# Kernel tuning notes

Hardware: AMD Instinct MI355X
Metric: run time of the kernel (lower is better)

## Reference

```python
import jax, jax.numpy as jnp
import numpy as np

NMS_RADIUS = 2.0   # cfgs.NMS_radius (meters)
EPS = 1e-6         # torch nn.PairwiseDistance default eps (added to the diff)
M = 16384          # number of keypoint candidates
SCENE = 100.0      # scene extent in meters


def setup_inputs() -> dict:
    key = jax.random.key(0)
    k1, k2 = jax.random.split(key)
    nodes = jax.random.uniform(k1, (M, 3), dtype=jnp.float32) * SCENE
    overlap_score = jax.random.normal(k2, (M,), dtype=jnp.float32)
    return {"nodes": nodes, "overlap_score": overlap_score}


def _greedy_nms(nodes, radius):
    """Sequential greedy NMS: keep node i iff its distance to every
    already-kept node exceeds radius. Faithful to the torch loop:
    (dis > radius).sum() == n_kept  <=>  all kept dists > radius."""
    n = nodes.shape[0]

    def body(i, mask):
        # torch nn.PairwiseDistance computes ||x1 - x2 + eps||_2
        d = jnp.linalg.norm(nodes[i] - nodes + EPS, axis=-1)  # [n]
        keep = jnp.all(jnp.where(mask, d > radius, True))
        return mask.at[i].set(keep)

    mask0 = jnp.zeros(n, dtype=bool).at[0].set(True)
    return jax.lax.fori_loop(1, n, body, mask0)


def reference(nodes, overlap_score):
    # sort by overlap score descending, run greedy NMS, unsort the mask
    order = jnp.argsort(-overlap_score)
    mask_sorted = _greedy_nms(nodes[order], NMS_RADIUS)
    mask = jnp.zeros_like(mask_sorted).at[order].set(mask_sorted)
    nms_length = mask.sum(dtype=jnp.int32)[None]
    return mask, nms_length
```

## Files before the change

kernel.cpp:

```cpp
#include <hip/hip_runtime.h>


#define M_PTS    16384
#define RADIUS   2.0f
#define EPS_D    1e-6f
#define GRID_N   25
#define NCELLS   (GRID_N * GRID_N * GRID_N)
#define CELL_CAP 12
#define K_NBR    12
#define EPT      5
#define ACT_PAD  (EPT * 1024)


__device__ __forceinline__ int cell_of(float v) {
  int c = (int)(v * 0.25f);
  return c < 0 ? 0 : (c > GRID_N - 1 ? GRID_N - 1 : c);
}

__global__ __launch_bounds__(256) void zero_kernel(int4* __restrict__ p) {
  int i = blockIdx.x * 256 + threadIdx.x;
  if (i < 8003) p[i] = make_int4(0, 0, 0, 0);
}

__global__ __launch_bounds__(256) void grid_build(
    const float* __restrict__ nodes, const float* __restrict__ score,
    float4* __restrict__ pts, int* __restrict__ cell_cnt,
    unsigned short* __restrict__ cell_list) {
  int i = blockIdx.x * 256 + threadIdx.x;
  if (i >= M_PTS) return;
  float4 p;
  p.x = nodes[3 * i + 0];
  p.y = nodes[3 * i + 1];
  p.z = nodes[3 * i + 2];
  p.w = score[i];
  pts[i] = p;
  int cid = (cell_of(p.x) * GRID_N + cell_of(p.y)) * GRID_N + cell_of(p.z);
  int pos = atomicAdd(&cell_cnt[cid], 1);
  if (pos < CELL_CAP) cell_list[cid * CELL_CAP + pos] = (unsigned short)i;
}

__global__ __launch_bounds__(256) void nbr_scan(
    const float4* __restrict__ pts, const int* __restrict__ cell_cnt,
    const unsigned short* __restrict__ cell_list,
    int* __restrict__ cnt, unsigned short* __restrict__ nbr) {
  int t = blockIdx.x * 256 + threadIdx.x;
  int i = t / 27;
  int d = t - i * 27;
  if (i >= M_PTS) return;
  const float4 pi = pts[i];
  int cx = cell_of(pi.x) + (d / 9) - 1;
  int cy = cell_of(pi.y) + ((d / 3) % 3) - 1;
  int cz = cell_of(pi.z) + (d % 3) - 1;
  if (cx < 0 || cx >= GRID_N || cy < 0 || cy >= GRID_N ||
      cz < 0 || cz >= GRID_N) return;
  int cid = (cx * GRID_N + cy) * GRID_N + cz;
  int m = cell_cnt[cid];
  if (m > CELL_CAP) m = CELL_CAP;
  for (int s = 0; s < m; ++s) {
    int j = cell_list[cid * CELL_CAP + s];
    float4 pj = pts[j];
    bool earlier = (pj.w > pi.w) || ((pj.w == pi.w) && (j < i));
    if (!earlier) continue;
    float ddx = __fadd_rn(__fsub_rn(pi.x, pj.x), EPS_D);
    float ddy = __fadd_rn(__fsub_rn(pi.y, pj.y), EPS_D);
    float ddz = __fadd_rn(__fsub_rn(pi.z, pj.z), EPS_D);
    float d2 = __fadd_rn(__fadd_rn(__fmul_rn(ddx, ddx), __fmul_rn(ddy, ddy)),
                         __fmul_rn(ddz, ddz));
    float dist = __fsqrt_rn(d2);
    if (!(dist > RADIUS)) {
      int pos = atomicAdd(&cnt[i], 1);
      if (pos < K_NBR) nbr[i * K_NBR + pos] = (unsigned short)j;
    }
  }
}

__global__ __launch_bounds__(1024) void solve_kernel(
    const int* __restrict__ cnt, const unsigned short* __restrict__ nbr,
    int* __restrict__ out, int out_size) {
  __shared__ unsigned char mask_[M_PTS];
  __shared__ unsigned int act[ACT_PAD];
  __shared__ int act_n, total;
  volatile unsigned char* mask = mask_;

  const int tid = threadIdx.x;
  const int lane = tid & 63;
  if (tid == 0) { act_n = 0; total = 0; }
  for (int a = tid; a < ACT_PAD; a += 1024) act[a] = 0u;
  __syncthreads();

  for (int k = tid; k < M_PTS; k += 1024) {
    mask_[k] = 1;
    int c = cnt[k];
    if (c > K_NBR) c = K_NBR;
    unsigned long long b = __ballot(c > 0);
    int wcnt = __popcll(b);
    int wbase = 0;
    if (lane == 0 && wcnt) wbase = atomicAdd(&act_n, wcnt);
    wbase = __shfl(wbase, 0, 64);
    if (c > 0) {
      int pos = wbase + __popcll(b & ((1ull << lane) - 1ull));
      if (pos < ACT_PAD) act[pos] = (unsigned)k | ((unsigned)c << 16);
    }
  }
  __syncthreads();
  const int na = act_n;
  const bool ok = (na <= ACT_PAD);

  unsigned ae[EPT];
  unsigned short r0[EPT], r1[EPT], r2[EPT];
#pragma unroll
  for (int e = 0; e < EPT; ++e) {
    unsigned v = act[tid + e * 1024];
    ae[e] = v;
    int k = (int)(v & 0xFFFFu);
    int c = (int)(v >> 16);
    const unsigned short* row = nbr + (size_t)k * K_NBR;
    r0[e] = (c > 0) ? row[0] : (unsigned short)0;
    r1[e] = (c > 1) ? row[1] : (unsigned short)0;
    r2[e] = (c > 2) ? row[2] : (unsigned short)0;
  }
  __syncthreads();

  if (ok) {
    for (int it = 0; it < 96; ++it) {
      int any = 0;
      int m0[EPT];
#pragma unroll
      for (int e = 0; e < EPT; ++e) m0[e] = (int)mask[r0[e]];
#pragma unroll
      for (int e = 0; e < EPT; ++e) {
        unsigned v = ae[e];
        int c = (int)(v >> 16);
        if (!c) continue;
        int k = (int)(v & 0xFFFFu);
        int kp = m0[e] ^ 1;
        if (c > 1) kp &= (int)mask[r1[e]] ^ 1;
        if (c > 2) kp &= (int)mask[r2[e]] ^ 1;
        if (c > 3) {
          const unsigned short* row = nbr + (size_t)k * K_NBR;
          for (int t = 3; t < c; ++t) kp &= (int)mask[row[t]] ^ 1;
        }
        if (kp != (int)mask[k]) { mask[k] = (unsigned char)kp; any = 1; }
      }
      if (__syncthreads_count(any) == 0) break;
    }
  } else {
    __shared__ int changed;
    for (int it = 0; it < 512; ++it) {
      if (tid == 0) changed = 0;
      __syncthreads();
      int any = 0;
      for (int k = tid; k < M_PTS; k += 1024) {
        int c = cnt[k]; if (c > K_NBR) c = K_NBR;
        if (!c) continue;
        int kp = 1;
        for (int t = 0; t < c; ++t) kp &= (int)mask[nbr[k * K_NBR + t]] ^ 1;
        if (kp != (int)mask[k]) { mask_[k] = (unsigned char)kp; any = 1; }
      }
      if (any) changed = 1;
      __syncthreads();
      if (!changed) break;
    }
  }
  __syncthreads();

  int ks = 0;
  for (int k = tid; k < M_PTS; k += 1024) {
    int m = (int)mask_[k];
    out[k] = m;
    ks += m;
  }
#pragma unroll
  for (int off = 32; off > 0; off >>= 1) ks += __shfl_down(ks, off, 64);
  if (lane == 0) atomicAdd(&total, ks);
  __syncthreads();
  if (tid == 0) out[out_size - 1] = total;
}

extern "C" void kernel_launch(void* const* d_in, const int* in_sizes, int n_in,
                              void* d_out, int out_size, void* d_ws, size_t ws_size,
                              hipStream_t stream) {
  const float* nodes = (const float*)d_in[0];
  const float* score = (const float*)d_in[1];
  int* out = (int*)d_out;

  char* ws = (char*)d_ws;
  float4* pts = (float4*)ws;
  int* cell_cnt = (int*)(ws + 262144);
  int* cnt = (int*)(ws + 324644);
  unsigned short* cell_list = (unsigned short*)(ws + 393216);
  unsigned short* nbr = (unsigned short*)(ws + 770048);

  zero_kernel<<<32, 256, 0, stream>>>((int4*)(ws + 262144));
  grid_build<<<64, 256, 0, stream>>>(nodes, score, pts, cell_cnt, cell_list);
  nbr_scan<<<1728, 256, 0, stream>>>(pts, cell_cnt, cell_list, cnt, nbr);
  solve_kernel<<<1, 1024, 0, stream>>>(cnt, nbr, out, out_size);
}
```

Baseline: 40.57 us.

## Fuse NMS pipeline into one cooperative kernel with grid syncs

Replaces the four launches (zero, grid build, neighbor scan, solve) with a single cooperative kernel of 256x512 threads that separates the phases with grid-wide syncs, removing launch gaps between kernels. Non-block-0 blocks write out[k]=1 for points that have no earlier neighbors, and block 0 solves and writes only the active points. Block 0 now holds 10 entries per thread over 512 threads. The multi-kernel path is kept as a fallback if the cooperative launch fails. Grid-sync cost and a lower-occupancy solve block may offset the launch savings.

Result: slower. 139.8 us (+244.7%).

```diff
diff --git a/kernel.cpp b/kernel.cpp
--- a/kernel.cpp
+++ b/kernel.cpp
@@ -1,4 +1,7 @@
 #include <hip/hip_runtime.h>
+#include <hip/hip_cooperative_groups.h>
+
+namespace cg = cooperative_groups;
 
 
 #define M_PTS    16384
@@ -8,14 +11,195 @@
 #define NCELLS   (GRID_N * GRID_N * GRID_N)
 #define CELL_CAP 12
 #define K_NBR    12
-#define EPT      5
-#define ACT_PAD  (EPT * 1024)
+#define NBLK     256
+#define NTHR     512
+#define EPT      10
+#define ACT_PAD  (EPT * NTHR)
+#define NTASK    (M_PTS * 27)
 
 
 __device__ __forceinline__ int cell_of(float v) {
   int c = (int)(v * 0.25f);
   return c < 0 ? 0 : (c > GRID_N - 1 ? GRID_N - 1 : c);
 }
+
+__device__ __forceinline__ bool edge_test(float4 pi, float4 pj, int j, int i) {
+  bool earlier = (pj.w > pi.w) || ((pj.w == pi.w) && (j < i));
+  if (!earlier) return false;
+  float ddx = __fadd_rn(__fsub_rn(pi.x, pj.x), EPS_D);
+  float ddy = __fadd_rn(__fsub_rn(pi.y, pj.y), EPS_D);
+  float ddz = __fadd_rn(__fsub_rn(pi.z, pj.z), EPS_D);
+  float d2 = __fadd_rn(__fadd_rn(__fmul_rn(ddx, ddx), __fmul_rn(ddy, ddy)),
+                       __fmul_rn(ddz, ddz));
+  return !(__fsqrt_rn(d2) > RADIUS);
+}
+
+__global__ __launch_bounds__(NTHR) void nms_fused(
+    const float* __restrict__ nodes, const float* __restrict__ score,
+    float4* __restrict__ pts, int* __restrict__ cell_cnt,
+    unsigned short* __restrict__ cell_list, int* __restrict__ cnt,
+    unsigned short* __restrict__ nbr, int* __restrict__ out, int out_size) {
+  __shared__ unsigned char mask_[M_PTS];
+  __shared__ unsigned int act[ACT_PAD];
+  __shared__ int act_n, total;
+  volatile unsigned char* mask = mask_;
+
+  cg::grid_group gg = cg::this_grid();
+  const int tid = threadIdx.x;
+  const int g   = blockIdx.x * NTHR + tid;
+  const int gsz = NBLK * NTHR;
+
+  for (int i = g; i < NCELLS + M_PTS; i += gsz) cell_cnt[i] = 0;
+  gg.sync();
+
+  if (g < M_PTS) {
+    float4 p;
+    p.x = nodes[3 * g + 0];
+    p.y = nodes[3 * g + 1];
+    p.z = nodes[3 * g + 2];
+    p.w = score[g];
+    pts[g] = p;
+    int cid = (cell_of(p.x) * GRID_N + cell_of(p.y)) * GRID_N + cell_of(p.z);
+    int pos = atomicAdd(&cell_cnt[cid], 1);
+    if (pos < CELL_CAP) cell_list[cid * CELL_CAP + pos] = (unsigned short)g;
+  }
+  gg.sync();
+
+  for (int t = g; t < NTASK; t += gsz) {
+    int i = t / 27;
+    int d = t - i * 27;
+    const float4 pi = pts[i];
+    int cx = cell_of(pi.x) + (d / 9) - 1;
+    int cy = cell_of(pi.y) + ((d / 3) % 3) - 1;
+    int cz = cell_of(pi.z) + (d % 3) - 1;
+    if (cx < 0 || cx >= GRID_N || cy < 0 || cy >= GRID_N ||
+        cz < 0 || cz >= GRID_N) continue;
+    int cid = (cx * GRID_N + cy) * GRID_N + cz;
+    int m = cell_cnt[cid];
+    if (m > CELL_CAP) m = CELL_CAP;
+    for (int s = 0; s < m; ++s) {
+      int j = cell_list[cid * CELL_CAP + s];
+      if (edge_test(pi, pts[j], j, i)) {
+        int pos = atomicAdd(&cnt[i], 1);
+        if (pos < K_NBR) nbr[i * K_NBR + pos] = (unsigned short)j;
+      }
+    }
+  }
+  gg.sync();
+
+  if (blockIdx.x != 0) {
+    int g2 = (blockIdx.x - 1) * NTHR + tid;
+    int gsz2 = (NBLK - 1) * NTHR;
+    for (int k = g2; k < M_PTS; k += gsz2)
+      if (cnt[k] == 0) out[k] = 1;
+    return;
+  }
+
+  const int lane = tid & 63;
+  if (tid == 0) { act_n = 0; total = 0; }
+  for (int a = tid; a < ACT_PAD; a += NTHR) act[a] = 0u;
+  __syncthreads();
+
+  for (int k = tid; k < M_PTS; k += NTHR) {
+    mask_[k] = 1;
+    int c = cnt[k];
+    if (c > K_NBR) c = K_NBR;
+    unsigned long long b = __ballot(c > 0);
+    int wcnt = __popcll(b);
+    int wbase = 0;
+    if (lane == 0 && wcnt) wbase = atomicAdd(&act_n, wcnt);
+    wbase = __shfl(wbase, 0, 64);
+    if (c > 0) {
+      int pos = wbase + __popcll(b & ((1ull << lane) - 1ull));
+      if (pos < ACT_PAD) act[pos] = (unsigned)k | ((unsigned)c << 16);
+    }
+  }
+  __syncthreads();
+  const int na = act_n;
+  const bool ok = (na <= ACT_PAD);
+
+  unsigned ae[EPT];
+  unsigned short r0[EPT], r1[EPT], r2[EPT];
+#pragma unroll
+  for (int e = 0; e < EPT; ++e) {
+    unsigned v = act[tid + e * NTHR];
+    ae[e] = v;
+    int k = (int)(v & 0xFFFFu);
+    int c = (int)(v >> 16);
+    const unsigned short* row = nbr + (size_t)k * K_NBR;
+    r0[e] = (c > 0) ? row[0] : (unsigned short)0;
+    r1[e] = (c > 1) ? row[1] : (unsigned short)0;
+    r2[e] = (c > 2) ? row[2] : (unsigned short)0;
+  }
+  __syncthreads();
+
+  if (ok) {
+    for (int it = 0; it < 96; ++it) {
+      int any = 0;
+      int m0[EPT];
+#pragma unroll
+      for (int e = 0; e < EPT; ++e) m0[e] = (int)mask[r0[e]];
+#pragma unroll
+      for (int e = 0; e < EPT; ++e) {
+        unsigned v = ae[e];
+        int c = (int)(v >> 16);
+        if (!c) continue;
+        int k = (int)(v & 0xFFFFu);
+        int kp = m0[e] ^ 1;
+        if (c > 1) kp &= (int)mask[r1[e]] ^ 1;
+        if (c > 2) kp &= (int)mask[r2[e]] ^ 1;
+        if (c > 3) {
+          const unsigned short* row = nbr + (size_t)k * K_NBR;
+          for (int t = 3; t < c; ++t) kp &= (int)mask[row[t]] ^ 1;
+        }
+        if (kp != (int)mask[k]) { mask[k] = (unsigned char)kp; any = 1; }
+      }
+      if (__syncthreads_count(any) == 0) break;
+    }
+    int ks = 0;
+    for (int a = tid; a < na; a += NTHR) {
+      int k = (int)(act[a] & 0xFFFFu);
+      int m = (int)mask_[k];
+      out[k] = m;
+      ks += m;
+    }
+#pragma unroll
+    for (int off = 32; off > 0; off >>= 1) ks += __shfl_down(ks, off, 64);
+    if (lane == 0) atomicAdd(&total, ks);
+    __syncthreads();
+    if (tid == 0) out[out_size - 1] = (M_PTS - na) + total;
+  } else {
+    __shared__ int changed;
+    for (int it = 0; it < 512; ++it) {
+      if (tid == 0) changed = 0;
+      __syncthreads();
+      int any = 0;
+      for (int k = tid; k < M_PTS; k += NTHR) {
+        int c = cnt[k]; if (c > K_NBR) c = K_NBR;
+        if (!c) continue;
+        int kp = 1;
+        for (int t = 0; t < c; ++t) kp &= (int)mask[nbr[k * K_NBR + t]] ^ 1;
+        if (kp != (int)mask[k]) { mask_[k] = (unsigned char)kp; any = 1; }
+      }
+      if (any) changed = 1;
+      __syncthreads();
+      if (!changed) break;
+    }
+    __syncthreads();
+    int ks = 0;
+    for (int k = tid; k < M_PTS; k += NTHR) {
+      int m = (int)mask_[k];
+      out[k] = m;
+      ks += m;
+    }
+#pragma unroll
+    for (int off = 32; off > 0; off >>= 1) ks += __shfl_down(ks, off, 64);
+    if (lane == 0) atomicAdd(&total, ks);
+    __syncthreads();
+    if (tid == 0) out[out_size - 1] = total;
+  }
+}
+
 
 __global__ __launch_bounds__(256) void zero_kernel(int4* __restrict__ p) {
   int i = blockIdx.x * 256 + threadIdx.x;
@@ -58,16 +242,7 @@
   if (m > CELL_CAP) m = CELL_CAP;
   for (int s = 0; s < m; ++s) {
     int j = cell_list[cid * CELL_CAP + s];
-    float4 pj = pts[j];
-    bool earlier = (pj.w > pi.w) || ((pj.w == pi.w) && (j < i));
-    if (!earlier) continue;
-    float ddx = __fadd_rn(__fsub_rn(pi.x, pj.x), EPS_D);
-    float ddy = __fadd_rn(__fsub_rn(pi.y, pj.y), EPS_D);
-    float ddz = __fadd_rn(__fsub_rn(pi.z, pj.z), EPS_D);
-    float d2 = __fadd_rn(__fadd_rn(__fmul_rn(ddx, ddx), __fmul_rn(ddy, ddy)),
-                         __fmul_rn(ddz, ddz));
-    float dist = __fsqrt_rn(d2);
-    if (!(dist > RADIUS)) {
+    if (edge_test(pi, pts[j], j, i)) {
       int pos = atomicAdd(&cnt[i], 1);
       if (pos < K_NBR) nbr[i * K_NBR + pos] = (unsigned short)j;
     }
@@ -106,10 +281,11 @@
   const int na = act_n;
   const bool ok = (na <= ACT_PAD);
 
-  unsigned ae[EPT];
-  unsigned short r0[EPT], r1[EPT], r2[EPT];
-#pragma unroll
-  for (int e = 0; e < EPT; ++e) {
+  const int FEPT = 5;
+  unsigned ae[FEPT];
+  unsigned short r0[FEPT], r1[FEPT], r2[FEPT];
+#pragma unroll
+  for (int e = 0; e < FEPT; ++e) {
     unsigned v = act[tid + e * 1024];
     ae[e] = v;
     int k = (int)(v & 0xFFFFu);
@@ -124,11 +300,11 @@
   if (ok) {
     for (int it = 0; it < 96; ++it) {
       int any = 0;
-      int m0[EPT];
-#pragma unroll
-      for (int e = 0; e < EPT; ++e) m0[e] = (int)mask[r0[e]];
-#pragma unroll
-      for (int e = 0; e < EPT; ++e) {
+      int m0[FEPT];
+#pragma unroll
+      for (int e = 0; e < FEPT; ++e) m0[e] = (int)mask[r0[e]];
+#pragma unroll
+      for (int e = 0; e < FEPT; ++e) {
         unsigned v = ae[e];
         int c = (int)(v >> 16);
         if (!c) continue;
@@ -191,8 +367,15 @@
   unsigned short* cell_list = (unsigned short*)(ws + 393216);
   unsigned short* nbr = (unsigned short*)(ws + 770048);
 
-  zero_kernel<<<32, 256, 0, stream>>>((int4*)(ws + 262144));
-  grid_build<<<64, 256, 0, stream>>>(nodes, score, pts, cell_cnt, cell_list);
-  nbr_scan<<<1728, 256, 0, stream>>>(pts, cell_cnt, cell_list, cnt, nbr);
-  solve_kernel<<<1, 1024, 0, stream>>>(cnt, nbr, out, out_size);
-}
+  void* args[] = {(void*)&nodes, (void*)&score, (void*)&pts, (void*)&cell_cnt,
+                  (void*)&cell_list, (void*)&cnt, (void*)&nbr, (void*)&out,
+                  (void*)&out_size};
+  hipError_t err = hipLaunchCooperativeKernel(
+      (const void*)nms_fused, dim3(NBLK), dim3(NTHR), args, 0, stream);
+  if (err != hipSuccess) {
+    zero_kernel<<<32, 256, 0, stream>>>((int4*)(ws + 262144));
+    grid_build<<<64, 256, 0, stream>>>(nodes, score, pts, cell_cnt, cell_list);
+    nbr_scan<<<1728, 256, 0, stream>>>(pts, cell_cnt, cell_list, cnt, nbr);
+    solve_kernel<<<1, 1024, 0, stream>>>(cnt, nbr, out, out_size);
+  }
+}
```

## Fuse four kernels into two with shared-memory grid build and last-block solve

Applied to the files above, without the earlier changes.

Removes the zero kernel by building the cell grid in a single block with shared-memory counters, then merges the neighbor scan and the greedy solve into one launch. The last block to finish, detected through an atomic done counter, runs the solve. The neighbor scan now gives each point a half-wave, with a prefix scan that writes neighbor lists without per-point global atomics. This cuts launch overhead and global atomics, at the cost of a serial single-block grid build, recomputing edge tests twice, and relying on threadfence and atomic ordering for correctness.

Result: slower. 89.23 us (+119.9%).

```diff
diff --git a/kernel.cpp b/kernel.cpp
--- a/kernel.cpp
+++ b/kernel.cpp
@@ -10,6 +10,10 @@
 #define K_NBR    12
 #define EPT      5
 #define ACT_PAD  (EPT * 1024)
+#define NBLK2    128
+#define NTHR2    1024
+#define WTASKS   (M_PTS / 2)
+#define GWAVES   (NBLK2 * NTHR2 / 64)
 
 
 __device__ __forceinline__ int cell_of(float v) {
@@ -17,88 +21,125 @@
   return c < 0 ? 0 : (c > GRID_N - 1 ? GRID_N - 1 : c);
 }
 
-__global__ __launch_bounds__(256) void zero_kernel(int4* __restrict__ p) {
-  int i = blockIdx.x * 256 + threadIdx.x;
-  if (i < 8003) p[i] = make_int4(0, 0, 0, 0);
-}
-
-__global__ __launch_bounds__(256) void grid_build(
+__device__ __forceinline__ bool edge_test(float4 pi, float4 pj, int j, int i) {
+  bool earlier = (pj.w > pi.w) || ((pj.w == pi.w) && (j < i));
+  if (!earlier) return false;
+  float ddx = __fadd_rn(__fsub_rn(pi.x, pj.x), EPS_D);
+  float ddy = __fadd_rn(__fsub_rn(pi.y, pj.y), EPS_D);
+  float ddz = __fadd_rn(__fsub_rn(pi.z, pj.z), EPS_D);
+  float d2 = __fadd_rn(__fadd_rn(__fmul_rn(ddx, ddx), __fmul_rn(ddy, ddy)),
+                       __fmul_rn(ddz, ddz));
+  return !(__fsqrt_rn(d2) > RADIUS);
+}
+
+__global__ __launch_bounds__(1024) void build1b(
     const float* __restrict__ nodes, const float* __restrict__ score,
     float4* __restrict__ pts, int* __restrict__ cell_cnt,
-    unsigned short* __restrict__ cell_list) {
-  int i = blockIdx.x * 256 + threadIdx.x;
-  if (i >= M_PTS) return;
-  float4 p;
-  p.x = nodes[3 * i + 0];
-  p.y = nodes[3 * i + 1];
-  p.z = nodes[3 * i + 2];
-  p.w = score[i];
-  pts[i] = p;
-  int cid = (cell_of(p.x) * GRID_N + cell_of(p.y)) * GRID_N + cell_of(p.z);
-  int pos = atomicAdd(&cell_cnt[cid], 1);
-  if (pos < CELL_CAP) cell_list[cid * CELL_CAP + pos] = (unsigned short)i;
-}
-
-__global__ __launch_bounds__(256) void nbr_scan(
+    unsigned short* __restrict__ cell_list, int* __restrict__ done) {
+  __shared__ int ccnt[NCELLS];
+  const int tid = threadIdx.x;
+  for (int c = tid; c < NCELLS; c += 1024) ccnt[c] = 0;
+  __syncthreads();
+  for (int i = tid; i < M_PTS; i += 1024) {
+    float4 p;
+    p.x = nodes[3 * i + 0];
+    p.y = nodes[3 * i + 1];
+    p.z = nodes[3 * i + 2];
+    p.w = score[i];
+    pts[i] = p;
+    int cid = (cell_of(p.x) * GRID_N + cell_of(p.y)) * GRID_N + cell_of(p.z);
+    int pos = atomicAdd(&ccnt[cid], 1);
+    if (pos < CELL_CAP) cell_list[cid * CELL_CAP + pos] = (unsigned short)i;
+  }
+  __syncthreads();
+  for (int c = tid; c < NCELLS; c += 1024) {
+    int v = ccnt[c];
+    cell_cnt[c] = v > CELL_CAP ? CELL_CAP : v;
+  }
+  if (tid == 0) *done = 0;
+}
+
+__global__ __launch_bounds__(NTHR2) void scan_solve(
     const float4* __restrict__ pts, const int* __restrict__ cell_cnt,
     const unsigned short* __restrict__ cell_list,
-    int* __restrict__ cnt, unsigned short* __restrict__ nbr) {
-  int t = blockIdx.x * 256 + threadIdx.x;
-  int i = t / 27;
-  int d = t - i * 27;
-  if (i >= M_PTS) return;
-  const float4 pi = pts[i];
-  int cx = cell_of(pi.x) + (d / 9) - 1;
-  int cy = cell_of(pi.y) + ((d / 3) % 3) - 1;
-  int cz = cell_of(pi.z) + (d % 3) - 1;
-  if (cx < 0 || cx >= GRID_N || cy < 0 || cy >= GRID_N ||
-      cz < 0 || cz >= GRID_N) return;
-  int cid = (cx * GRID_N + cy) * GRID_N + cz;
-  int m = cell_cnt[cid];
-  if (m > CELL_CAP) m = CELL_CAP;
-  for (int s = 0; s < m; ++s) {
-    int j = cell_list[cid * CELL_CAP + s];
-    float4 pj = pts[j];
-    bool earlier = (pj.w > pi.w) || ((pj.w == pi.w) && (j < i));
-    if (!earlier) continue;
-    float ddx = __fadd_rn(__fsub_rn(pi.x, pj.x), EPS_D);
-    float ddy = __fadd_rn(__fsub_rn(pi.y, pj.y), EPS_D);
-    float ddz = __fadd_rn(__fsub_rn(pi.z, pj.z), EPS_D);
-    float d2 = __fadd_rn(__fadd_rn(__fmul_rn(ddx, ddx), __fmul_rn(ddy, ddy)),
-                         __fmul_rn(ddz, ddz));
-    float dist = __fsqrt_rn(d2);
-    if (!(dist > RADIUS)) {
-      int pos = atomicAdd(&cnt[i], 1);
-      if (pos < K_NBR) nbr[i * K_NBR + pos] = (unsigned short)j;
-    }
-  }
-}
-
-__global__ __launch_bounds__(1024) void solve_kernel(
-    const int* __restrict__ cnt, const unsigned short* __restrict__ nbr,
-    int* __restrict__ out, int out_size) {
+    int* __restrict__ cnt, unsigned short* __restrict__ nbr,
+    int* __restrict__ done, int* __restrict__ out, int out_size) {
   __shared__ unsigned char mask_[M_PTS];
   __shared__ unsigned int act[ACT_PAD];
-  __shared__ int act_n, total;
+  __shared__ int act_n, total, islast;
   volatile unsigned char* mask = mask_;
 
-  const int tid = threadIdx.x;
+  const int tid  = threadIdx.x;
   const int lane = tid & 63;
+  const int d    = lane & 31;
+  const int half = lane >> 5;
+  const int gwave = (blockIdx.x * NTHR2 + tid) >> 6;
+
+  for (int wt = gwave; wt < WTASKS; wt += GWAVES) {
+    int i = wt * 2 + half;
+    float4 pi = pts[i];
+    int n = 0, cid = 0, m = 0;
+    if (d < 27) {
+      int cx = cell_of(pi.x) + d / 9 - 1;
+      int cy = cell_of(pi.y) + (d / 3) % 3 - 1;
+      int cz = cell_of(pi.z) + d % 3 - 1;
+      if (cx >= 0 && cx < GRID_N && cy >= 0 && cy < GRID_N &&
+          cz >= 0 && cz < GRID_N) {
+        cid = (cx * GRID_N + cy) * GRID_N + cz;
+        m = cell_cnt[cid];
+        for (int s = 0; s < m; ++s) {
+          int j = cell_list[cid * CELL_CAP + s];
+          if (edge_test(pi, pts[j], j, i)) ++n;
+        }
+      }
+    }
+    int x = n;
+#pragma unroll
+    for (int off = 1; off < 32; off <<= 1) {
+      int y = __shfl_up(x, off, 32);
+      if (d >= off) x += y;
+    }
+    int excl = x - n;
+    int tot = __shfl(x, 31, 32);
+    if (n > 0) {
+      int pos = excl;
+      for (int s = 0; s < m && pos < K_NBR; ++s) {
+        int j = cell_list[cid * CELL_CAP + s];
+        if (edge_test(pi, pts[j], j, i)) {
+          nbr[i * K_NBR + pos] = (unsigned short)j;
+          ++pos;
+        }
+      }
+    }
+    if (d == 0) cnt[i] = tot > K_NBR ? K_NBR : tot;
+  }
+
+  __syncthreads();
+  __threadfence();
+  if (tid == 0) {
+    int old = atomicAdd(done, 1);
+    islast = (old == NBLK2 - 1);
+  }
+  __syncthreads();
+  if (!islast) return;
+  __threadfence();
+
+  const int lane64 = lane;
   if (tid == 0) { act_n = 0; total = 0; }
-  for (int a = tid; a < ACT_PAD; a += 1024) act[a] = 0u;
-  __syncthreads();
-
-  for (int k = tid; k < M_PTS; k += 1024) {
+  for (int a = tid; a < ACT_PAD; a += NTHR2) act[a] = 0u;
+  __syncthreads();
+
+  for (int k = tid; k < M_PTS; k += NTHR2) {
     mask_[k] = 1;
     int c = cnt[k];
     if (c > K_NBR) c = K_NBR;
     unsigned long long b = __ballot(c > 0);
     int wcnt = __popcll(b);
     int wbase = 0;
-    if (lane == 0 && wcnt) wbase = atomicAdd(&act_n, wcnt);
+    if (lane64 == 0 && wcnt) wbase = atomicAdd(&act_n, wcnt);
     wbase = __shfl(wbase, 0, 64);
     if (c > 0) {
-      int pos = wbase + __popcll(b & ((1ull << lane) - 1ull));
+      int pos = wbase + __popcll(b & ((1ull << lane64) - 1ull));
       if (pos < ACT_PAD) act[pos] = (unsigned)k | ((unsigned)c << 16);
     }
   }
@@ -110,7 +151,7 @@
   unsigned short r0[EPT], r1[EPT], r2[EPT];
 #pragma unroll
   for (int e = 0; e < EPT; ++e) {
-    unsigned v = act[tid + e * 1024];
+    unsigned v = act[tid + e * NTHR2];
     ae[e] = v;
     int k = (int)(v & 0xFFFFu);
     int c = (int)(v >> 16);
@@ -150,7 +191,7 @@
       if (tid == 0) changed = 0;
       __syncthreads();
       int any = 0;
-      for (int k = tid; k < M_PTS; k += 1024) {
+      for (int k = tid; k < M_PTS; k += NTHR2) {
         int c = cnt[k]; if (c > K_NBR) c = K_NBR;
         if (!c) continue;
         int kp = 1;
@@ -165,14 +206,14 @@
   __syncthreads();
 
   int ks = 0;
-  for (int k = tid; k < M_PTS; k += 1024) {
+  for (int k = tid; k < M_PTS; k += NTHR2) {
     int m = (int)mask_[k];
     out[k] = m;
     ks += m;
   }
 #pragma unroll
   for (int off = 32; off > 0; off >>= 1) ks += __shfl_down(ks, off, 64);
-  if (lane == 0) atomicAdd(&total, ks);
+  if (lane64 == 0) atomicAdd(&total, ks);
   __syncthreads();
   if (tid == 0) out[out_size - 1] = total;
 }
@@ -187,12 +228,12 @@
   char* ws = (char*)d_ws;
   float4* pts = (float4*)ws;
   int* cell_cnt = (int*)(ws + 262144);
-  int* cnt = (int*)(ws + 324644);
+  int* done = (int*)(ws + 324644);
+  int* cnt = (int*)(ws + 327680);
   unsigned short* cell_list = (unsigned short*)(ws + 393216);
   unsigned short* nbr = (unsigned short*)(ws + 770048);
 
-  zero_kernel<<<32, 256, 0, stream>>>((int4*)(ws + 262144));
-  grid_build<<<64, 256, 0, stream>>>(nodes, score, pts, cell_cnt, cell_list);
-  nbr_scan<<<1728, 256, 0, stream>>>(pts, cell_cnt, cell_list, cnt, nbr);
-  solve_kernel<<<1, 1024, 0, stream>>>(cnt, nbr, out, out_size);
-}
+  build1b<<<1, 1024, 0, stream>>>(nodes, score, pts, cell_cnt, cell_list, done);
+  scan_solve<<<NBLK2, NTHR2, 0, stream>>>(pts, cell_cnt, cell_list, cnt, nbr,
+                                          done, out, out_size);
+}
```

## Fuse grid build and neighbor scan into per-block redundant binning kernel

Applied to the files above, without the earlier changes.

Replaces the zero, grid-build and neighbor-scan kernels with a single kernel of 16 blocks. Each block rebuilds the full cell grid in shared memory, then scans neighbors for its own slice of points and writes a compacted active list with the first three neighbors packed in. The solve kernel gathers these partial lists instead of rescanning all counts, and writes outputs only for active points, with isolated points written directly by the first kernel. This removes two launches and the global atomics, at the price of each block repeating the binning of all 16384 points and reduced parallelism in the scan phase.

New measurement: 87.42 us. +115.5%, slower.

```diff
diff --git a/kernel.cpp b/kernel.cpp
--- a/kernel.cpp
+++ b/kernel.cpp
@@ -8,120 +8,164 @@
 #define NCELLS   (GRID_N * GRID_N * GRID_N)
 #define CELL_CAP 12
 #define K_NBR    12
-#define EPT      5
-#define ACT_PAD  (EPT * 1024)
-
+#define NBLK1    16
+#define PPB      (M_PTS / NBLK1)
+#define ACT_PAD  6144
+#define EPT      6
+
+#define LIST_STRIDE_E 187520
+#define ACT_STRIDE_W  (1024 * 3)
 
 __device__ __forceinline__ int cell_of(float v) {
   int c = (int)(v * 0.25f);
   return c < 0 ? 0 : (c > GRID_N - 1 ? GRID_N - 1 : c);
 }
 
-__global__ __launch_bounds__(256) void zero_kernel(int4* __restrict__ p) {
-  int i = blockIdx.x * 256 + threadIdx.x;
-  if (i < 8003) p[i] = make_int4(0, 0, 0, 0);
-}
-
-__global__ __launch_bounds__(256) void grid_build(
+__device__ __forceinline__ bool edge_test(float xi, float yi, float zi, float si,
+                                          float xj, float yj, float zj, float sj,
+                                          int j, int i) {
+  bool earlier = (sj > si) || ((sj == si) && (j < i));
+  if (!earlier) return false;
+  float ddx = __fadd_rn(__fsub_rn(xi, xj), EPS_D);
+  float ddy = __fadd_rn(__fsub_rn(yi, yj), EPS_D);
+  float ddz = __fadd_rn(__fsub_rn(zi, zj), EPS_D);
+  float d2 = __fadd_rn(__fadd_rn(__fmul_rn(ddx, ddx), __fmul_rn(ddy, ddy)),
+                       __fmul_rn(ddz, ddz));
+  return !(__fsqrt_rn(d2) > RADIUS);
+}
+
+__global__ __launch_bounds__(1024) void bin_scan(
     const float* __restrict__ nodes, const float* __restrict__ score,
-    float4* __restrict__ pts, int* __restrict__ cell_cnt,
-    unsigned short* __restrict__ cell_list) {
-  int i = blockIdx.x * 256 + threadIdx.x;
-  if (i >= M_PTS) return;
-  float4 p;
-  p.x = nodes[3 * i + 0];
-  p.y = nodes[3 * i + 1];
-  p.z = nodes[3 * i + 2];
-  p.w = score[i];
-  pts[i] = p;
-  int cid = (cell_of(p.x) * GRID_N + cell_of(p.y)) * GRID_N + cell_of(p.z);
-  int pos = atomicAdd(&cell_cnt[cid], 1);
-  if (pos < CELL_CAP) cell_list[cid * CELL_CAP + pos] = (unsigned short)i;
-}
-
-__global__ __launch_bounds__(256) void nbr_scan(
-    const float4* __restrict__ pts, const int* __restrict__ cell_cnt,
-    const unsigned short* __restrict__ cell_list,
-    int* __restrict__ cnt, unsigned short* __restrict__ nbr) {
-  int t = blockIdx.x * 256 + threadIdx.x;
-  int i = t / 27;
-  int d = t - i * 27;
-  if (i >= M_PTS) return;
-  const float4 pi = pts[i];
-  int cx = cell_of(pi.x) + (d / 9) - 1;
-  int cy = cell_of(pi.y) + ((d / 3) % 3) - 1;
-  int cz = cell_of(pi.z) + (d % 3) - 1;
-  if (cx < 0 || cx >= GRID_N || cy < 0 || cy >= GRID_N ||
-      cz < 0 || cz >= GRID_N) return;
-  int cid = (cx * GRID_N + cy) * GRID_N + cz;
-  int m = cell_cnt[cid];
-  if (m > CELL_CAP) m = CELL_CAP;
-  for (int s = 0; s < m; ++s) {
-    int j = cell_list[cid * CELL_CAP + s];
-    float4 pj = pts[j];
-    bool earlier = (pj.w > pi.w) || ((pj.w == pi.w) && (j < i));
-    if (!earlier) continue;
-    float ddx = __fadd_rn(__fsub_rn(pi.x, pj.x), EPS_D);
-    float ddy = __fadd_rn(__fsub_rn(pi.y, pj.y), EPS_D);
-    float ddz = __fadd_rn(__fsub_rn(pi.z, pj.z), EPS_D);
-    float d2 = __fadd_rn(__fadd_rn(__fmul_rn(ddx, ddx), __fmul_rn(ddy, ddy)),
-                         __fmul_rn(ddz, ddz));
-    float dist = __fsqrt_rn(d2);
-    if (!(dist > RADIUS)) {
-      int pos = atomicAdd(&cnt[i], 1);
-      if (pos < K_NBR) nbr[i * K_NBR + pos] = (unsigned short)j;
-    }
-  }
-}
-
-__global__ __launch_bounds__(1024) void solve_kernel(
-    const int* __restrict__ cnt, const unsigned short* __restrict__ nbr,
-    int* __restrict__ out, int out_size) {
+    unsigned short* __restrict__ lists, unsigned int* __restrict__ act_part,
+    int* __restrict__ cnt_part, unsigned short* __restrict__ nbr,
+    int* __restrict__ out) {
+  __shared__ int ccnt[NCELLS];
+  __shared__ int nact;
+  const int tid = threadIdx.x;
+  const int b   = blockIdx.x;
+  unsigned short* mylist = lists + (size_t)b * LIST_STRIDE_E;
+
+  for (int c = tid; c < NCELLS; c += 1024) ccnt[c] = 0;
+  if (tid == 0) nact = 0;
+  __syncthreads();
+
+  for (int i = tid; i < M_PTS; i += 1024) {
+    float x = nodes[3 * i + 0];
+    float y = nodes[3 * i + 1];
+    float z = nodes[3 * i + 2];
+    int cid = (cell_of(x) * GRID_N + cell_of(y)) * GRID_N + cell_of(z);
+    int pos = atomicAdd(&ccnt[cid], 1);
+    if (pos < CELL_CAP) mylist[cid * CELL_CAP + pos] = (unsigned short)i;
+  }
+  __syncthreads();
+
+  const int i = b * PPB + tid;
+  const float xi = nodes[3 * i + 0];
+  const float yi = nodes[3 * i + 1];
+  const float zi = nodes[3 * i + 2];
+  const float si = score[i];
+  const int cx = cell_of(xi), cy = cell_of(yi), cz = cell_of(zi);
+  unsigned short row[3] = {0, 0, 0};
+  int n = 0;
+  for (int dx = -1; dx <= 1; ++dx) {
+    int x = cx + dx; if (x < 0 || x >= GRID_N) continue;
+    for (int dy = -1; dy <= 1; ++dy) {
+      int y = cy + dy; if (y < 0 || y >= GRID_N) continue;
+      for (int dz = -1; dz <= 1; ++dz) {
+        int z = cz + dz; if (z < 0 || z >= GRID_N) continue;
+        int cid = (x * GRID_N + y) * GRID_N + z;
+        int m = ccnt[cid]; if (m > CELL_CAP) m = CELL_CAP;
+        for (int s = 0; s < m; ++s) {
+          int j = mylist[cid * CELL_CAP + s];
+          float xj = nodes[3 * j + 0];
+          float yj = nodes[3 * j + 1];
+          float zj = nodes[3 * j + 2];
+          float sj = score[j];
+          if (edge_test(xi, yi, zi, si, xj, yj, zj, sj, j, i)) {
+            if (n < 3)     row[n] = (unsigned short)j;
+            if (n < K_NBR) nbr[i * K_NBR + n] = (unsigned short)j;
+            ++n;
+          }
+        }
+      }
+    }
+  }
+  int c = n > K_NBR ? K_NBR : n;
+  if (c == 0) out[i] = 1;
+
+  unsigned long long bal = __ballot(c > 0);
+  const int lane = tid & 63;
+  int wcnt = __popcll(bal);
+  int wbase = 0;
+  if (lane == 0 && wcnt) wbase = atomicAdd(&nact, wcnt);
+  wbase = __shfl(wbase, 0, 64);
+  if (c > 0) {
+    int pos = wbase + __popcll(bal & ((1ull << lane) - 1ull));
+    unsigned int* e = act_part + (size_t)b * ACT_STRIDE_W + (size_t)pos * 3;
+    e[0] = (unsigned)i | ((unsigned)c << 16);
+    e[1] = (unsigned)row[0] | ((unsigned)row[1] << 16);
+    e[2] = (unsigned)row[2];
+  }
+  __syncthreads();
+  if (tid == 0) cnt_part[b] = nact;
+}
+
+__global__ __launch_bounds__(1024) void solve2(
+    const unsigned int* __restrict__ act_part, const int* __restrict__ cnt_part,
+    const unsigned short* __restrict__ nbr, int* __restrict__ out, int out_size) {
   __shared__ unsigned char mask_[M_PTS];
-  __shared__ unsigned int act[ACT_PAD];
-  __shared__ int act_n, total;
+  __shared__ unsigned int a0[ACT_PAD];
+  __shared__ unsigned int a1[ACT_PAD];
+  __shared__ unsigned int a2[ACT_PAD];
+  __shared__ int offs[NBLK1 + 1];
+  __shared__ int cpart[NBLK1];
+  __shared__ int total;
   volatile unsigned char* mask = mask_;
 
   const int tid = threadIdx.x;
   const int lane = tid & 63;
-  if (tid == 0) { act_n = 0; total = 0; }
-  for (int a = tid; a < ACT_PAD; a += 1024) act[a] = 0u;
-  __syncthreads();
-
-  for (int k = tid; k < M_PTS; k += 1024) {
-    mask_[k] = 1;
-    int c = cnt[k];
-    if (c > K_NBR) c = K_NBR;
-    unsigned long long b = __ballot(c > 0);
-    int wcnt = __popcll(b);
-    int wbase = 0;
-    if (lane == 0 && wcnt) wbase = atomicAdd(&act_n, wcnt);
-    wbase = __shfl(wbase, 0, 64);
-    if (c > 0) {
-      int pos = wbase + __popcll(b & ((1ull << lane) - 1ull));
-      if (pos < ACT_PAD) act[pos] = (unsigned)k | ((unsigned)c << 16);
-    }
-  }
-  __syncthreads();
-  const int na = act_n;
+
+  for (int k = tid; k < M_PTS; k += 1024) mask_[k] = 1;
+  if (tid < NBLK1) cpart[tid] = cnt_part[tid];
+  if (tid == 0) total = 0;
+  __syncthreads();
+  if (tid == 0) {
+    int acc = 0;
+    for (int bb = 0; bb < NBLK1; ++bb) { offs[bb] = acc; acc += cpart[bb]; }
+    offs[NBLK1] = acc;
+  }
+  __syncthreads();
+  const int na = offs[NBLK1];
   const bool ok = (na <= ACT_PAD);
 
-  unsigned ae[EPT];
-  unsigned short r0[EPT], r1[EPT], r2[EPT];
-#pragma unroll
-  for (int e = 0; e < EPT; ++e) {
-    unsigned v = act[tid + e * 1024];
-    ae[e] = v;
-    int k = (int)(v & 0xFFFFu);
-    int c = (int)(v >> 16);
-    const unsigned short* row = nbr + (size_t)k * K_NBR;
-    r0[e] = (c > 0) ? row[0] : (unsigned short)0;
-    r1[e] = (c > 1) ? row[1] : (unsigned short)0;
-    r2[e] = (c > 2) ? row[2] : (unsigned short)0;
-  }
-  __syncthreads();
-
   if (ok) {
+    for (int bb = 0; bb < NBLK1; ++bb) {
+      int base = offs[bb], nb = offs[bb + 1] - base;
+      const unsigned int* src = act_part + (size_t)bb * ACT_STRIDE_W;
+      for (int e = tid; e < nb; e += 1024) {
+        a0[base + e] = src[e * 3 + 0];
+        a1[base + e] = src[e * 3 + 1];
+        a2[base + e] = src[e * 3 + 2];
+      }
+    }
+    for (int e = na + tid; e < ACT_PAD; e += 1024) { a0[e] = 0; a1[e] = 0; a2[e] = 0; }
+  }
+  __syncthreads();
+
+  if (ok) {
+    unsigned ae[EPT];
+    unsigned short r0[EPT], r1[EPT], r2[EPT];
+#pragma unroll
+    for (int e = 0; e < EPT; ++e) {
+      int idx = tid + e * 1024;
+      ae[e] = a0[idx];
+      unsigned w1 = a1[idx], w2 = a2[idx];
+      r0[e] = (unsigned short)(w1 & 0xFFFFu);
+      r1[e] = (unsigned short)(w1 >> 16);
+      r2[e] = (unsigned short)(w2 & 0xFFFFu);
+    }
+    __syncthreads();
+
     for (int it = 0; it < 96; ++it) {
       int any = 0;
       int m0[EPT];
@@ -137,44 +181,67 @@
         if (c > 1) kp &= (int)mask[r1[e]] ^ 1;
         if (c > 2) kp &= (int)mask[r2[e]] ^ 1;
         if (c > 3) {
-          const unsigned short* row = nbr + (size_t)k * K_NBR;
-          for (int t = 3; t < c; ++t) kp &= (int)mask[row[t]] ^ 1;
+          const unsigned short* rowp = nbr + (size_t)k * K_NBR;
+          for (int t = 3; t < c; ++t) kp &= (int)mask[rowp[t]] ^ 1;
         }
         if (kp != (int)mask[k]) { mask[k] = (unsigned char)kp; any = 1; }
       }
       if (__syncthreads_count(any) == 0) break;
     }
+
+    int ks = 0;
+    for (int e = tid; e < na; e += 1024) {
+      int k = (int)(a0[e] & 0xFFFFu);
+      int m = (int)mask_[k];
+      out[k] = m;
+      ks += m;
+    }
+#pragma unroll
+    for (int off = 32; off > 0; off >>= 1) ks += __shfl_down(ks, off, 64);
+    if (lane == 0) atomicAdd(&total, ks);
+    __syncthreads();
+    if (tid == 0) out[out_size - 1] = (M_PTS - na) + total;
   } else {
     __shared__ int changed;
     for (int it = 0; it < 512; ++it) {
       if (tid == 0) changed = 0;
       __syncthreads();
       int any = 0;
-      for (int k = tid; k < M_PTS; k += 1024) {
-        int c = cnt[k]; if (c > K_NBR) c = K_NBR;
-        if (!c) continue;
-        int kp = 1;
-        for (int t = 0; t < c; ++t) kp &= (int)mask[nbr[k * K_NBR + t]] ^ 1;
-        if (kp != (int)mask[k]) { mask_[k] = (unsigned char)kp; any = 1; }
+      for (int bb = 0; bb < NBLK1; ++bb) {
+        int nb = cpart[bb];
+        const unsigned int* src = act_part + (size_t)bb * ACT_STRIDE_W;
+        for (int e = tid; e < nb; e += 1024) {
+          unsigned v = src[e * 3 + 0];
+          int k = (int)(v & 0xFFFFu);
+          int c = (int)(v >> 16);
+          int kp = 1;
+          const unsigned short* rowp = nbr + (size_t)k * K_NBR;
+          for (int t = 0; t < c; ++t) kp &= (int)mask[rowp[t]] ^ 1;
+          if (kp != (int)mask[k]) { mask_[k] = (unsigned char)kp; any = 1; }
+        }
       }
       if (any) changed = 1;
       __syncthreads();
       if (!changed) break;
     }
-  }
-  __syncthreads();
-
-  int ks = 0;
-  for (int k = tid; k < M_PTS; k += 1024) {
-    int m = (int)mask_[k];
-    out[k] = m;
-    ks += m;
-  }
-#pragma unroll
-  for (int off = 32; off > 0; off >>= 1) ks += __shfl_down(ks, off, 64);
-  if (lane == 0) atomicAdd(&total, ks);
-  __syncthreads();
-  if (tid == 0) out[out_size - 1] = total;
+    __syncthreads();
+    int ks = 0;
+    for (int bb = 0; bb < NBLK1; ++bb) {
+      int nb = cpart[bb];
+      const unsigned int* src = act_part + (size_t)bb * ACT_STRIDE_W;
+      for (int e = tid; e < nb; e += 1024) {
+        int k = (int)(src[e * 3] & 0xFFFFu);
+        int m = (int)mask_[k];
+        out[k] = m;
+        ks += m;
+      }
+    }
+#pragma unroll
+    for (int off = 32; off > 0; off >>= 1) ks += __shfl_down(ks, off, 64);
+    if (lane == 0) atomicAdd(&total, ks);
+    __syncthreads();
+    if (tid == 0) out[out_size - 1] = (M_PTS - na) + total;
+  }
 }
 
 extern "C" void kernel_launch(void* const* d_in, const int* in_sizes, int n_in,
@@ -185,14 +252,12 @@
   int* out = (int*)d_out;
 
   char* ws = (char*)d_ws;
-  float4* pts = (float4*)ws;
-  int* cell_cnt = (int*)(ws + 262144);
-  int* cnt = (int*)(ws + 324644);
-  unsigned short* cell_list = (unsigned short*)(ws + 393216);
-  unsigned short* nbr = (unsigned short*)(ws + 770048);
-
-  zero_kernel<<<32, 256, 0, stream>>>((int4*)(ws + 262144));
-  grid_build<<<64, 256, 0, stream>>>(nodes, score, pts, cell_cnt, cell_list);
-  nbr_scan<<<1728, 256, 0, stream>>>(pts, cell_cnt, cell_list, cnt, nbr);
-  solve_kernel<<<1, 1024, 0, stream>>>(cnt, nbr, out, out_size);
-}
+  unsigned short* nbr = (unsigned short*)ws;
+  int* cnt_part = (int*)(ws + 393216);
+  unsigned int* act_part = (unsigned int*)(ws + 397312);
+  unsigned short* lists = (unsigned short*)(ws + 1048576);
+
+  bin_scan<<<NBLK1, 1024, 0, stream>>>(nodes, score, lists, act_part,
+                                       cnt_part, nbr, out);
+  solve2<<<1, 1024, 0, stream>>>(act_part, cnt_part, nbr, out, out_size);
+}
```
